# Kernel tuning notes

Hardware: AMD Instinct MI355X
Metric: run time of the kernel (lower is better)

The kernel has to match this reference:

```python
import jax, jax.numpy as jnp
import numpy as np

EPS = 1e-6


def _gru_cell(x, h, w_ih, w_hh, b_ih, b_hh):
    # PyTorch GRU gate order: r, z, n
    gi = x @ w_ih.T + b_ih          # (B, 3H)
    gh = h @ w_hh.T + b_hh          # (B, 3H)
    ir, iz, inn = jnp.split(gi, 3, axis=-1)
    hr, hz, hn = jnp.split(gh, 3, axis=-1)
    r = jax.nn.sigmoid(ir + hr)
    z = jax.nn.sigmoid(iz + hz)
    n = jnp.tanh(inn + r * hn)
    return (1.0 - z) * n + z * h


def setup_inputs() -> dict:
    key = jax.random.key(0)
    B, C, H, O = 32768, 512, 256, 2
    ks = jax.random.split(key, 16)
    s_ih0 = 1.0 / np.sqrt(H)
    inp = {
        "context": jax.random.normal(ks[0], (B, C), dtype=jnp.float32),
        "pred_len": 60,
        "w_init": jax.random.normal(ks[1], (H * 2, C), dtype=jnp.float32) * (1.0 / np.sqrt(C)),
        "b_init": jnp.zeros((H * 2,), dtype=jnp.float32),
        "w_ih0": jax.random.normal(ks[2], (3 * H, O + C), dtype=jnp.float32) * s_ih0,
        "w_hh0": jax.random.normal(ks[3], (3 * H, H), dtype=jnp.float32) * s_ih0,
        "b_ih0": jax.random.normal(ks[4], (3 * H,), dtype=jnp.float32) * s_ih0,
        "b_hh0": jax.random.normal(ks[5], (3 * H,), dtype=jnp.float32) * s_ih0,
        "w_ih1": jax.random.normal(ks[6], (3 * H, H), dtype=jnp.float32) * s_ih0,
        "w_hh1": jax.random.normal(ks[7], (3 * H, H), dtype=jnp.float32) * s_ih0,
        "b_ih1": jax.random.normal(ks[8], (3 * H,), dtype=jnp.float32) * s_ih0,
        "b_hh1": jax.random.normal(ks[9], (3 * H,), dtype=jnp.float32) * s_ih0,
        "w_pos": jax.random.normal(ks[10], (O, H), dtype=jnp.float32) * s_ih0,
        "b_pos": jnp.zeros((O,), dtype=jnp.float32),
        "w_chol": jax.random.normal(ks[11], (3, H), dtype=jnp.float32) * s_ih0,
        "b_chol": jnp.zeros((3,), dtype=jnp.float32),
    }
    return inp


def reference(context, pred_len, w_init, b_init,
              w_ih0, w_hh0, b_ih0, b_hh0,
              w_ih1, w_hh1, b_ih1, b_hh1,
              w_pos, b_pos, w_chol, b_chol):
    B = context.shape[0]
    H = w_hh0.shape[1]
    # init hidden: tanh(W_init c + b), split into per-layer states
    hid = jnp.tanh(context @ w_init.T + b_init)       # (B, 2H)
    h0, h1 = hid[:, :H], hid[:, H:]
    pos0 = jnp.zeros((B, w_pos.shape[0]), dtype=context.dtype)
    zeros = jnp.zeros((B,), dtype=context.dtype)

    def step(carry, _):
        h0, h1, pos = carry
        x = jnp.concatenate([pos, context], axis=1)   # (B, O+C)
        h0 = _gru_cell(x, h0, w_ih0, w_hh0, b_ih0, b_hh0)
        h1 = _gru_cell(h0, h1, w_ih1, w_hh1, b_ih1, b_hh1)
        pred = h1 @ w_pos.T + b_pos                   # (B, 2)
        z = h1 @ w_chol.T + b_chol                    # (B, 3)
        l11 = jax.nn.softplus(z[:, 0]) + EPS
        l21 = z[:, 1]
        l22 = jax.nn.softplus(z[:, 2]) + EPS
        L = jnp.stack([jnp.stack([l11, zeros], axis=-1),
                       jnp.stack([l21, l22], axis=-1)], axis=-2)  # (B, 2, 2)
        return (h0, h1, pred), (pred, L)

    _, (preds, Ls) = jax.lax.scan(step, (h0, h1, pos0), None, length=pred_len)
    predictions = jnp.transpose(preds, (1, 0, 2))     # (B, T, 2)
    cholesky = jnp.transpose(Ls, (1, 0, 2, 3))        # (B, T, 2, 2)
    return predictions, cholesky
```

## Files before the change

### kernel.cpp

```cpp
#include <hip/hip_runtime.h>
#include <hip/hip_bf16.h>
#include <cstdint>
#include <cstddef>


typedef __attribute__((ext_vector_type(8)))  short bf16x8;
typedef __attribute__((ext_vector_type(16))) float f32x16;
typedef __attribute__((ext_vector_type(4)))  float f32x4;
typedef unsigned short ushort_t;
typedef unsigned int   uint32;

#define MFMA_BF16(A,B,C) __builtin_amdgcn_mfma_f32_32x32x16_bf16(A,B,C,0,0,0)
#define MMA3(ACC, AH, AL, BH, BL)            \
  ACC = MFMA_BF16(AH, BH, ACC);              \
  ACC = MFMA_BF16(AH, BL, ACC);              \
  ACC = MFMA_BF16(AL, BH, ACC);

#define TSTEPS 60
#define CB_OFF 3932160

#define WPK0 0u
#define WPK1 786432u
#define WPK2 1572864u
#define WPKI 2359296u
#define WPKG 3407872u
#define JCON 4980736u
#define OUTW 4993024u
#define NTWO 5001216u

#define OFF_H0 0
#define OFF_H1 65536
#define OFF_BUF 131072
#define OFF_POS 147456
#define SMEM_BYTES 147968

__device__ __forceinline__ ushort_t f2bf(float x){
  uint32 u = __builtin_bit_cast(uint32, x);
  u += 0x7fffu + ((u >> 16) & 1u);
  return (ushort_t)(u >> 16);
}
__device__ __forceinline__ float bf2f(ushort_t b){
  uint32 u = ((uint32)b) << 16;
  return __builtin_bit_cast(float, u);
}
__device__ __forceinline__ void zero16(f32x16& a){
  #pragma unroll
  for (int i=0;i<16;i++) a[i] = 0.f;
}

#define LOG2E 1.44269504088896340736f
#define LN2   0.69314718055994530942f
__device__ __forceinline__ float fexp2(float x){ return __builtin_amdgcn_exp2f(x); }
__device__ __forceinline__ float flog2(float x){ return __builtin_amdgcn_logf(x); }
__device__ __forceinline__ float frcp (float x){ return __builtin_amdgcn_rcpf(x); }
__device__ __forceinline__ float fsig(float x){ return frcp(1.f + fexp2(-LOG2E*x)); }
__device__ __forceinline__ float ftanh(float x){
  float ax = fabsf(x);
  float e  = fexp2(-2.f*LOG2E*ax);
  float t  = (1.f - e)*frcp(1.f + e);
  return copysignf(t, x);
}
__device__ __forceinline__ float fsoftplus(float x){
  float ax = fabsf(x);
  return fmaxf(x, 0.f) + LN2*flog2(1.f + fexp2(-LOG2E*ax));
}

__device__ __forceinline__ void pack_unit(const float* __restrict__ src, int stride, int colOff,
                                          char* __restrict__ dst, int NC, int ncLog, int v)
{
  int l = v & 63;
  int c = (v >> 6) & (NC-1);
  int t = v >> (6 + ncLog);
  int j  = 32*t + (l & 31);
  int k0 = 16*c + ((l >> 5) << 3);
  const float* s = src + (size_t)j*stride + colOff + k0;
  uint32 hp[4], lp[4];
  #pragma unroll
  for (int i=0;i<4;i++){
    float x0 = s[2*i], x1 = s[2*i+1];
    ushort_t h0_ = f2bf(x0), h1_ = f2bf(x1);
    ushort_t l0_ = f2bf(x0 - bf2f(h0_)), l1_ = f2bf(x1 - bf2f(h1_));
    hp[i] = (uint32)h0_ | ((uint32)h1_ << 16);
    lp[i] = (uint32)l0_ | ((uint32)l1_ << 16);
  }
  char* d = dst + ((size_t)(t*NC + c))*2048 + (size_t)l*16;
  *(uint4*)d          = make_uint4(hp[0],hp[1],hp[2],hp[3]);
  *(uint4*)(d + 1024) = make_uint4(lp[0],lp[1],lp[2],lp[3]);
}

__global__ void k_pack(const float* __restrict__ w_init, const float* __restrict__ w_ih0,
                       const float* __restrict__ w_hh0, const float* __restrict__ b_hh0,
                       const float* __restrict__ w_ih1, const float* __restrict__ w_hh1,
                       const float* __restrict__ b_ih1, const float* __restrict__ b_hh1,
                       const float* __restrict__ w_pos, const float* __restrict__ w_chol,
                       char* __restrict__ ws)
{
  int u = blockIdx.x*256 + threadIdx.x;
  if (u < 73728){
    int seg = u / 24576; int v = u % 24576;
    const float* src = (seg==0) ? w_hh0 : ((seg==1) ? w_ih1 : w_hh1);
    char* dst = ws + ((seg==0) ? WPK0 : ((seg==1) ? WPK1 : WPK2));
    pack_unit(src, 256, 0, dst, 16, 4, v);
  } else if (u < 106496){
    pack_unit(w_init, 512, 0, ws + WPKI, 32, 5, u - 73728);
  } else if (u < 155648){
    pack_unit(w_ih0, 514, 2, ws + WPKG, 32, 5, u - 106496);
  } else if (u < 156416){
    int j = u - 155648;
    float w4 = (j < 512) ? (b_ih1[j] + b_hh1[j]) : b_ih1[j];
    ((float4*)(ws + JCON))[j] =
        make_float4(b_hh0[j], w_ih0[(size_t)j*514 + 0], w_ih0[(size_t)j*514 + 1], w4);
  } else if (u < 156672){
    int k = u - 156416;
    ((float4*)(ws + OUTW))[2*k]   = make_float4(w_pos[k], w_pos[256+k], w_chol[k], w_chol[256+k]);
    ((float4*)(ws + OUTW))[2*k+1] = make_float4(w_chol[512+k], 0.f, 0.f, 0.f);
  } else if (u < 156928){
    int k = u - 156672;
    ((float*)(ws + NTWO))[k] = b_hh1[512+k];
  }
}


template<int NTILE, int NCHUNK>
__device__ __forceinline__ void gemm_frag(const char* __restrict__ apk, int w, int l,
                                          const char* __restrict__ sbase,
                                          f32x16 (&acc)[NTILE][2])
{
  #pragma unroll 4
  for (int c=0;c<NCHUNK;c++){
    bf16x8 A[NTILE][2];
    #pragma unroll
    for (int i=0;i<NTILE;i++){
      const char* p = apk + ((size_t)((w+8*i)*NCHUNK + c))*2048 + (size_t)l*16;
      A[i][0] = *(const bf16x8*)p;
      A[i][1] = *(const bf16x8*)(p + 1024);
    }
    bf16x8 Bf[2][2];
    #pragma unroll
    for (int s=0;s<2;s++)
      #pragma unroll
      for (int p2=0;p2<2;p2++)
        Bf[s][p2] = *(const bf16x8*)(sbase + ((c*2+p2)*2+s)*1024 + l*16);
    #pragma unroll
    for (int i=0;i<NTILE;i++)
      #pragma unroll
      for (int s=0;s<2;s++){
        MMA3(acc[i][s], A[i][0], A[i][1], Bf[s][0], Bf[s][1]);
      }
  }
}

__device__ __forceinline__ void readback(const char* __restrict__ hbase, int w, int l,
                                         f32x16 (&ho)[2])
{
  const int L = l >> 5, l31 = l & 31;
  #pragma unroll
  for (int s=0;s<2;s++)
    #pragma unroll
    for (int g=0;g<4;g++){
      int cg = 2*w + (g>>1);
      int lane2 = l31 + 32*(g&1);
      const char* ph = hbase + ((cg*2+0)*2 + s)*1024 + lane2*16 + 8*L;
      const char* pl = hbase + ((cg*2+1)*2 + s)*1024 + lane2*16 + 8*L;
      uint2 hb = *(const uint2*)ph;
      uint2 lb = *(const uint2*)pl;
      ho[s][4*g+0] = bf2f((ushort_t)(hb.x & 0xffff)) + bf2f((ushort_t)(lb.x & 0xffff));
      ho[s][4*g+1] = bf2f((ushort_t)(hb.x >> 16))    + bf2f((ushort_t)(lb.x >> 16));
      ho[s][4*g+2] = bf2f((ushort_t)(hb.y & 0xffff)) + bf2f((ushort_t)(lb.y & 0xffff));
      ho[s][4*g+3] = bf2f((ushort_t)(hb.y >> 16))    + bf2f((ushort_t)(lb.y >> 16));
    }
}

__device__ __forceinline__ void write_state(char* __restrict__ hbase, int w, int l,
                                            const f32x16 (&hn)[2])
{
  const int L = l >> 5;
  #pragma unroll
  for (int s=0;s<2;s++){
    float loc[16], sw[16];
    #pragma unroll
    for (int q=0;q<16;q++){ loc[q] = hn[s][q]; sw[q] = __shfl_xor(loc[q], 32, 64); }
    #pragma unroll
    for (int c=0;c<2;c++){
      float v[8];
      if (L == 0){
        #pragma unroll
        for (int r=0;r<8;r++){ int q = (r&3) + 8*c;     v[r] = (r<4)  ? loc[q] : sw[q]; }
      } else {
        #pragma unroll
        for (int r=0;r<8;r++){ int q = (r&3) + 8*c + 4; v[r] = (r>=4) ? loc[q] : sw[q]; }
      }
      uint32 hp[4], lp[4];
      #pragma unroll
      for (int i=0;i<4;i++){
        ushort_t h0_ = f2bf(v[2*i]), h1_ = f2bf(v[2*i+1]);
        ushort_t l0_ = f2bf(v[2*i] - bf2f(h0_)), l1_ = f2bf(v[2*i+1] - bf2f(h1_));
        hp[i] = (uint32)h0_ | ((uint32)h1_ << 16);
        lp[i] = (uint32)l0_ | ((uint32)l1_ << 16);
      }
      int cg = 2*w + c;
      *(uint4*)(hbase + ((cg*2+0)*2+s)*1024 + l*16) = make_uint4(hp[0],hp[1],hp[2],hp[3]);
      *(uint4*)(hbase + ((cg*2+1)*2+s)*1024 + l*16) = make_uint4(lp[0],lp[1],lp[2],lp[3]);
    }
  }
}

__global__ __launch_bounds__(512, 2) void decoder_main(
    const float* __restrict__ ctx,
    const float* __restrict__ b_init,
    const float* __restrict__ b_ih0,
    const float* __restrict__ b_pos,
    const float* __restrict__ b_chol,
    const char*  __restrict__ ws,
    float*       __restrict__ out)
{
  extern __shared__ char smem[];
  const int tid = threadIdx.x;
  const int w   = tid >> 6;
  const int l   = tid & 63;
  const int L   = l >> 5;
  const int l31 = l & 31;
  const int blk = blockIdx.x;
  const int B0  = blk * 64;
  const float4* jconst = (const float4*)(ws + JCON);
  const float4* outw   = (const float4*)(ws + OUTW);
  const float*  n2c    = (const float*)(ws + NTWO);
  float* posb = (float*)(smem + OFF_POS);
  float* buff = (float*)(smem + OFF_BUF);

  #pragma unroll
  for (int ci=0; ci<4; ci++){
    int c = w + 8*ci;
    #pragma unroll
    for (int s=0;s<2;s++){
      const float* src = ctx + (size_t)(B0 + 32*s + l31)*512 + 16*c + 8*L;
      float4 a0 = *(const float4*)src;
      float4 a1 = *(const float4*)(src + 4);
      float xs[8] = {a0.x,a0.y,a0.z,a0.w,a1.x,a1.y,a1.z,a1.w};
      uint32 hp[4], lp[4];
      #pragma unroll
      for (int i=0;i<4;i++){
        ushort_t h0_ = f2bf(xs[2*i]), h1_ = f2bf(xs[2*i+1]);
        ushort_t l0_ = f2bf(xs[2*i] - bf2f(h0_)), l1_ = f2bf(xs[2*i+1] - bf2f(h1_));
        hp[i] = (uint32)h0_ | ((uint32)h1_ << 16);
        lp[i] = (uint32)l0_ | ((uint32)l1_ << 16);
      }
      *(uint4*)(smem + ((c*2+0)*2 + s)*1024 + l*16) = make_uint4(hp[0],hp[1],hp[2],hp[3]);
      *(uint4*)(smem + ((c*2+1)*2 + s)*1024 + l*16) = make_uint4(lp[0],lp[1],lp[2],lp[3]);
    }
  }
  __syncthreads();

  f32x16 hD0[2], hD1[2];
  {
    f32x16 aH[2][2];
    zero16(aH[0][0]); zero16(aH[0][1]); zero16(aH[1][0]); zero16(aH[1][1]);
    gemm_frag<2,32>(ws + WPKI, w, l, smem, aH);
    #pragma unroll
    for (int ti=0; ti<2; ti++)
      #pragma unroll
      for (int s=0;s<2;s++)
        #pragma unroll
        for (int g=0;g<4;g++)
          #pragma unroll
          for (int e=0;e<4;e++){
            int kq = 4*L + e + 8*g;
            int j  = 32*(w + 8*ti) + kq;
            float v = ftanh(aH[ti][s][4*g+e] + b_init[j]);
            if (ti==0) hD0[s][4*g+e] = v; else hD1[s][4*g+e] = v;
          }
  }

  f32x16 gi[3][2];
  {
    #pragma unroll
    for (int i=0;i<3;i++){ zero16(gi[i][0]); zero16(gi[i][1]); }
    gemm_frag<3,32>(ws + WPKG, w, l, smem, gi);
    #pragma unroll
    for (int ti=0; ti<3; ti++)
      #pragma unroll
      for (int s=0;s<2;s++)
        #pragma unroll
        for (int g=0;g<4;g++)
          #pragma unroll
          for (int e=0;e<4;e++){
            int kq = 4*L + e + 8*g;
            int j  = 32*(w + 8*ti) + kq;
            gi[ti][s][4*g+e] += b_ih0[j];
          }
  }
  __syncthreads();

  write_state(smem + OFF_H0, w, l, hD0);
  write_state(smem + OFF_H1, w, l, hD1);
  if (tid < 128) posb[tid] = 0.f;
  __syncthreads();

  for (int t=0; t<TSTEPS; t++){
    f32x16 g0[3][2];
    #pragma unroll
    for (int i=0;i<3;i++){ zero16(g0[i][0]); zero16(g0[i][1]); }
    gemm_frag<3,16>(ws + WPK0, w, l, smem + OFF_H0, g0);

    f32x16 ho[2];
    readback(smem + OFF_H0, w, l, ho);
    float p0v[2], p1v[2];
    #pragma unroll
    for (int s=0;s<2;s++){
      float2 pp = *(const float2*)(posb + (32*s + l31)*2);
      p0v[s] = pp.x; p1v[s] = pp.y;
    }

    f32x16 hn0[2];
    #pragma unroll
    for (int g=0;g<4;g++)
      #pragma unroll
      for (int e=0;e<4;e++){
        int kq = 4*L + e + 8*g;
        int jr = 32*w + kq;
        float4 jcr = jconst[jr], jcz = jconst[256+jr], jcn = jconst[512+jr];
        #pragma unroll
        for (int s=0;s<2;s++){
          int q = 4*g + e;
          float gi_r = gi[0][s][q] + jcr.y*p0v[s] + jcr.z*p1v[s];
          float gi_z = gi[1][s][q] + jcz.y*p0v[s] + jcz.z*p1v[s];
          float gi_n = gi[2][s][q] + jcn.y*p0v[s] + jcn.z*p1v[s];
          float r = fsig(gi_r + g0[0][s][q] + jcr.x);
          float z = fsig(gi_z + g0[1][s][q] + jcz.x);
          float n = ftanh(gi_n + r*(g0[2][s][q] + jcn.x));
          hn0[s][q] = (1.f - z)*n + z*ho[s][q];
        }
      }
    __syncthreads();
    write_state(smem + OFF_H0, w, l, hn0);
    __syncthreads();

    f32x16 aR[2], aZ[2], aNi[2], aNh[2];
    zero16(aR[0]); zero16(aR[1]); zero16(aZ[0]); zero16(aZ[1]);
    zero16(aNi[0]); zero16(aNi[1]); zero16(aNh[0]); zero16(aNh[1]);
    {
      const char* pk1 = ws + WPK1;
      const char* pk2 = ws + WPK2;
      #pragma unroll 4
      for (int c=0;c<16;c++){
        bf16x8 A1[3][2], A2[3][2];
        #pragma unroll
        for (int i=0;i<3;i++){
          size_t o = ((size_t)((w+8*i)*16 + c))*2048 + (size_t)l*16;
          A1[i][0] = *(const bf16x8*)(pk1+o); A1[i][1] = *(const bf16x8*)(pk1+o+1024);
          A2[i][0] = *(const bf16x8*)(pk2+o); A2[i][1] = *(const bf16x8*)(pk2+o+1024);
        }
        bf16x8 B0f[2][2], B1f[2][2];
        #pragma unroll
        for (int s=0;s<2;s++)
          #pragma unroll
          for (int p2=0;p2<2;p2++){
            B0f[s][p2] = *(const bf16x8*)(smem + OFF_H0 + ((c*2+p2)*2+s)*1024 + l*16);
            B1f[s][p2] = *(const bf16x8*)(smem + OFF_H1 + ((c*2+p2)*2+s)*1024 + l*16);
          }
        #pragma unroll
        for (int s=0;s<2;s++){
          MMA3(aR[s],  A1[0][0], A1[0][1], B0f[s][0], B0f[s][1]);
          MMA3(aR[s],  A2[0][0], A2[0][1], B1f[s][0], B1f[s][1]);
          MMA3(aZ[s],  A1[1][0], A1[1][1], B0f[s][0], B0f[s][1]);
          MMA3(aZ[s],  A2[1][0], A2[1][1], B1f[s][0], B1f[s][1]);
          MMA3(aNi[s], A1[2][0], A1[2][1], B0f[s][0], B0f[s][1]);
          MMA3(aNh[s], A2[2][0], A2[2][1], B1f[s][0], B1f[s][1]);
        }
      }
    }

    f32x16 h1o[2];
    readback(smem + OFF_H1, w, l, h1o);
    f32x16 hn1[2];
    #pragma unroll
    for (int g=0;g<4;g++)
      #pragma unroll
      for (int e=0;e<4;e++){
        int kq = 4*L + e + 8*g;
        int k  = 32*w + kq;
        float4 jcr = jconst[k], jcz = jconst[256+k], jcn = jconst[512+k];
        float nb = n2c[k];
        #pragma unroll
        for (int s=0;s<2;s++){
          int q = 4*g + e;
          float r = fsig(aR[s][q] + jcr.w);
          float z = fsig(aZ[s][q] + jcz.w);
          float n = ftanh(aNi[s][q] + jcn.w + r*(aNh[s][q] + nb));
          hn1[s][q] = (1.f - z)*n + z*h1o[s][q];
        }
      }
    __syncthreads();
    write_state(smem + OFF_H1, w, l, hn1);

    float part[2][5];
    #pragma unroll
    for (int s=0;s<2;s++){ part[s][0]=part[s][1]=part[s][2]=part[s][3]=part[s][4]=0.f; }
    #pragma unroll
    for (int g=0;g<4;g++)
      #pragma unroll
      for (int e=0;e<4;e++){
        int kq = 4*L + e + 8*g;
        int k  = 32*w + kq;
        float4 o0 = outw[2*k], o1 = outw[2*k+1];
        #pragma unroll
        for (int s=0;s<2;s++){
          float h = hn1[s][4*g+e];
          part[s][0] += h*o0.x; part[s][1] += h*o0.y; part[s][2] += h*o0.z;
          part[s][3] += h*o0.w; part[s][4] += h*o1.x;
        }
      }
    #pragma unroll
    for (int s=0;s<2;s++)
      #pragma unroll
      for (int o=0;o<5;o++)
        part[s][o] += __shfl_xor(part[s][o], 32, 64);
    if (l < 32){
      #pragma unroll
      for (int s=0;s<2;s++){
        float* bp = buff + (size_t)(w*64 + 32*s + l)*8;
        bp[0]=part[s][0]; bp[1]=part[s][1]; bp[2]=part[s][2]; bp[3]=part[s][3]; bp[4]=part[s][4];
      }
    }
    __syncthreads();

    if (tid < 320){
      int b = tid / 5, o = tid - 5*b;
      float v = 0.f;
      #pragma unroll
      for (int w8=0; w8<8; w8++) v += buff[(size_t)(w8*64 + b)*8 + o];
      int gb = B0 + b;
      if (o < 2){
        float pr = v + b_pos[o];
        out[(size_t)gb*120 + t*2 + o] = pr;
        posb[b*2 + o] = pr;
      } else if (o == 2){
        float l11 = fsoftplus(v + b_chol[0]) + 1e-6f;
        out[CB_OFF + (size_t)gb*240 + t*4 + 0] = l11;
        out[CB_OFF + (size_t)gb*240 + t*4 + 1] = 0.f;
      } else if (o == 3){
        out[CB_OFF + (size_t)gb*240 + t*4 + 2] = v + b_chol[1];
      } else {
        out[CB_OFF + (size_t)gb*240 + t*4 + 3] = fsoftplus(v + b_chol[2]) + 1e-6f;
      }
    }
    __syncthreads();
  }
}

extern "C" void kernel_launch(void* const* d_in, const int* in_sizes, int n_in,
                              void* d_out, int out_size, void* d_ws, size_t ws_size,
                              hipStream_t stream)
{
  const float* ctx    = (const float*)d_in[0];
  const float* w_init = (const float*)d_in[2];
  const float* b_init = (const float*)d_in[3];
  const float* w_ih0  = (const float*)d_in[4];
  const float* w_hh0  = (const float*)d_in[5];
  const float* b_ih0  = (const float*)d_in[6];
  const float* b_hh0  = (const float*)d_in[7];
  const float* w_ih1  = (const float*)d_in[8];
  const float* w_hh1  = (const float*)d_in[9];
  const float* b_ih1  = (const float*)d_in[10];
  const float* b_hh1  = (const float*)d_in[11];
  const float* w_pos  = (const float*)d_in[12];
  const float* b_pos  = (const float*)d_in[13];
  const float* w_chol = (const float*)d_in[14];
  const float* b_chol = (const float*)d_in[15];
  char*  ws  = (char*)d_ws;
  float* out = (float*)d_out;

  hipFuncSetAttribute((const void*)decoder_main,
                      hipFuncAttributeMaxDynamicSharedMemorySize, SMEM_BYTES);

  k_pack<<<613, 256, 0, stream>>>(w_init, w_ih0, w_hh0, b_hh0, w_ih1, w_hh1,
                                  b_ih1, b_hh1, w_pos, w_chol, ws);
  decoder_main<<<512, 512, SMEM_BYTES, stream>>>(ctx, b_init, b_ih0, b_pos, b_chol,
                                                 ws, out);
}
```

Measured before the change: 13.17 ms.

## Pack loop-invariant input gates to fp16 and split layer-1 GEMM to cut registers

The precomputed input-gate accumulators (gi), which live in registers across all timesteps, are now stored as packed fp16 pairs, halving their register footprint. The layer-1 recurrent GEMM is split into two passes: r/z gates first, whose sigmoid outputs are packed to fp16, then the n-gate accumulators. This lowers peak accumulator liveness. Unroll factors drop from 4 to 2 to further reduce register pressure, likely aiming to avoid spills or raise occupancy. In exchange it adds fp16 rounding of the gate values, extra pack/unpack work, and a second pass over the hidden state in LDS.

```diff
diff --git a/kernel.cpp b/kernel.cpp
--- a/kernel.cpp
+++ b/kernel.cpp
@@ -1,5 +1,6 @@
 #include <hip/hip_runtime.h>
 #include <hip/hip_bf16.h>
+#include <hip/hip_fp16.h>
 #include <cstdint>
 #include <cstddef>
 
@@ -46,6 +47,15 @@
 __device__ __forceinline__ void zero16(f32x16& a){
   #pragma unroll
   for (int i=0;i<16;i++) a[i] = 0.f;
+}
+__device__ __forceinline__ uint32 packh2(float a, float b){
+  ushort_t ua = __builtin_bit_cast(ushort_t, __float2half_rn(a));
+  ushort_t ub = __builtin_bit_cast(ushort_t, __float2half_rn(b));
+  return (uint32)ua | ((uint32)ub << 16);
+}
+__device__ __forceinline__ float unph(uint32 p, int hiHalf){
+  ushort_t u = (ushort_t)(hiHalf ? (p >> 16) : (p & 0xffffu));
+  return __half2float(__builtin_bit_cast(__half, u));
 }
 
 #define LOG2E 1.44269504088896340736f
@@ -126,7 +136,7 @@
                                           const char* __restrict__ sbase,
                                           f32x16 (&acc)[NTILE][2])
 {
-  #pragma unroll 4
+  #pragma unroll 2
   for (int c=0;c<NCHUNK;c++){
     bf16x8 A[NTILE][2];
     #pragma unroll
@@ -251,6 +261,27 @@
   }
   __syncthreads();
 
+  uint32 giP[3][2][8];
+  {
+    f32x16 aG[3][2];
+    #pragma unroll
+    for (int i=0;i<3;i++){ zero16(aG[i][0]); zero16(aG[i][1]); }
+    gemm_frag<3,32>(ws + WPKG, w, l, smem, aG);
+    #pragma unroll
+    for (int ti=0; ti<3; ti++)
+      #pragma unroll
+      for (int s=0;s<2;s++)
+        #pragma unroll
+        for (int j=0;j<8;j++){
+          int q0 = 2*j, q1 = 2*j+1;
+          int kq0 = 4*L + (q0&3) + 8*(q0>>2);
+          int kq1 = 4*L + (q1&3) + 8*(q1>>2);
+          float v0 = aG[ti][s][q0] + b_ih0[32*(w+8*ti) + kq0];
+          float v1 = aG[ti][s][q1] + b_ih0[32*(w+8*ti) + kq1];
+          giP[ti][s][j] = packh2(v0, v1);
+        }
+  }
+
   f32x16 hD0[2], hD1[2];
   {
     f32x16 aH[2][2];
@@ -270,25 +301,6 @@
             if (ti==0) hD0[s][4*g+e] = v; else hD1[s][4*g+e] = v;
           }
   }
-
-  f32x16 gi[3][2];
-  {
-    #pragma unroll
-    for (int i=0;i<3;i++){ zero16(gi[i][0]); zero16(gi[i][1]); }
-    gemm_frag<3,32>(ws + WPKG, w, l, smem, gi);
-    #pragma unroll
-    for (int ti=0; ti<3; ti++)
-      #pragma unroll
-      for (int s=0;s<2;s++)
-        #pragma unroll
-        for (int g=0;g<4;g++)
-          #pragma unroll
-          for (int e=0;e<4;e++){
-            int kq = 4*L + e + 8*g;
-            int j  = 32*(w + 8*ti) + kq;
-            gi[ti][s][4*g+e] += b_ih0[j];
-          }
-  }
   __syncthreads();
 
   write_state(smem + OFF_H0, w, l, hD0);
@@ -318,13 +330,13 @@
       for (int e=0;e<4;e++){
         int kq = 4*L + e + 8*g;
         int jr = 32*w + kq;
+        int q  = 4*g + e;
         float4 jcr = jconst[jr], jcz = jconst[256+jr], jcn = jconst[512+jr];
         #pragma unroll
         for (int s=0;s<2;s++){
-          int q = 4*g + e;
-          float gi_r = gi[0][s][q] + jcr.y*p0v[s] + jcr.z*p1v[s];
-          float gi_z = gi[1][s][q] + jcz.y*p0v[s] + jcz.z*p1v[s];
-          float gi_n = gi[2][s][q] + jcn.y*p0v[s] + jcn.z*p1v[s];
+          float gi_r = unph(giP[0][s][q>>1], q&1) + jcr.y*p0v[s] + jcr.z*p1v[s];
+          float gi_z = unph(giP[1][s][q>>1], q&1) + jcz.y*p0v[s] + jcz.z*p1v[s];
+          float gi_n = unph(giP[2][s][q>>1], q&1) + jcn.y*p0v[s] + jcn.z*p1v[s];
           float r = fsig(gi_r + g0[0][s][q] + jcr.x);
           float z = fsig(gi_z + g0[1][s][q] + jcz.x);
           float n = ftanh(gi_n + r*(g0[2][s][q] + jcn.x));
@@ -335,17 +347,17 @@
     write_state(smem + OFF_H0, w, l, hn0);
     __syncthreads();
 
-    f32x16 aR[2], aZ[2], aNi[2], aNh[2];
-    zero16(aR[0]); zero16(aR[1]); zero16(aZ[0]); zero16(aZ[1]);
-    zero16(aNi[0]); zero16(aNi[1]); zero16(aNh[0]); zero16(aNh[1]);
+    uint32 rP[2][8], zP[2][8];
     {
+      f32x16 aR[2], aZ[2];
+      zero16(aR[0]); zero16(aR[1]); zero16(aZ[0]); zero16(aZ[1]);
       const char* pk1 = ws + WPK1;
       const char* pk2 = ws + WPK2;
-      #pragma unroll 4
+      #pragma unroll 2
       for (int c=0;c<16;c++){
-        bf16x8 A1[3][2], A2[3][2];
-        #pragma unroll
-        for (int i=0;i<3;i++){
+        bf16x8 A1[2][2], A2[2][2];
+        #pragma unroll
+        for (int i=0;i<2;i++){
           size_t o = ((size_t)((w+8*i)*16 + c))*2048 + (size_t)l*16;
           A1[i][0] = *(const bf16x8*)(pk1+o); A1[i][1] = *(const bf16x8*)(pk1+o+1024);
           A2[i][0] = *(const bf16x8*)(pk2+o); A2[i][1] = *(const bf16x8*)(pk2+o+1024);
@@ -360,36 +372,77 @@
           }
         #pragma unroll
         for (int s=0;s<2;s++){
-          MMA3(aR[s],  A1[0][0], A1[0][1], B0f[s][0], B0f[s][1]);
-          MMA3(aR[s],  A2[0][0], A2[0][1], B1f[s][0], B1f[s][1]);
-          MMA3(aZ[s],  A1[1][0], A1[1][1], B0f[s][0], B0f[s][1]);
-          MMA3(aZ[s],  A2[1][0], A2[1][1], B1f[s][0], B1f[s][1]);
-          MMA3(aNi[s], A1[2][0], A1[2][1], B0f[s][0], B0f[s][1]);
-          MMA3(aNh[s], A2[2][0], A2[2][1], B1f[s][0], B1f[s][1]);
-        }
-      }
-    }
-
-    f32x16 h1o[2];
-    readback(smem + OFF_H1, w, l, h1o);
+          MMA3(aR[s], A1[0][0], A1[0][1], B0f[s][0], B0f[s][1]);
+          MMA3(aR[s], A2[0][0], A2[0][1], B1f[s][0], B1f[s][1]);
+          MMA3(aZ[s], A1[1][0], A1[1][1], B0f[s][0], B0f[s][1]);
+          MMA3(aZ[s], A2[1][0], A2[1][1], B1f[s][0], B1f[s][1]);
+        }
+      }
+      #pragma unroll
+      for (int s=0;s<2;s++)
+        #pragma unroll
+        for (int j=0;j<8;j++){
+          int q0 = 2*j, q1 = 2*j+1;
+          int k0 = 32*w + 4*L + (q0&3) + 8*(q0>>2);
+          int k1 = 32*w + 4*L + (q1&3) + 8*(q1>>2);
+          float r0 = fsig(aR[s][q0] + jconst[k0].w);
+          float r1 = fsig(aR[s][q1] + jconst[k1].w);
+          float z0 = fsig(aZ[s][q0] + jconst[256+k0].w);
+          float z1 = fsig(aZ[s][q1] + jconst[256+k1].w);
+          rP[s][j] = packh2(r0, r1);
+          zP[s][j] = packh2(z0, z1);
+        }
+    }
+
     f32x16 hn1[2];
-    #pragma unroll
-    for (int g=0;g<4;g++)
-      #pragma unroll
-      for (int e=0;e<4;e++){
-        int kq = 4*L + e + 8*g;
-        int k  = 32*w + kq;
-        float4 jcr = jconst[k], jcz = jconst[256+k], jcn = jconst[512+k];
-        float nb = n2c[k];
+    {
+      f32x16 aNi[2], aNh[2];
+      zero16(aNi[0]); zero16(aNi[1]); zero16(aNh[0]); zero16(aNh[1]);
+      const char* pk1 = ws + WPK1;
+      const char* pk2 = ws + WPK2;
+      #pragma unroll 2
+      for (int c=0;c<16;c++){
+        bf16x8 A1f[2], A2f[2];
+        {
+          size_t o = ((size_t)((w+16)*16 + c))*2048 + (size_t)l*16;
+          A1f[0] = *(const bf16x8*)(pk1+o); A1f[1] = *(const bf16x8*)(pk1+o+1024);
+          A2f[0] = *(const bf16x8*)(pk2+o); A2f[1] = *(const bf16x8*)(pk2+o+1024);
+        }
+        bf16x8 B0f[2][2], B1f[2][2];
+        #pragma unroll
+        for (int s=0;s<2;s++)
+          #pragma unroll
+          for (int p2=0;p2<2;p2++){
+            B0f[s][p2] = *(const bf16x8*)(smem + OFF_H0 + ((c*2+p2)*2+s)*1024 + l*16);
+            B1f[s][p2] = *(const bf16x8*)(smem + OFF_H1 + ((c*2+p2)*2+s)*1024 + l*16);
+          }
         #pragma unroll
         for (int s=0;s<2;s++){
-          int q = 4*g + e;
-          float r = fsig(aR[s][q] + jcr.w);
-          float z = fsig(aZ[s][q] + jcz.w);
-          float n = ftanh(aNi[s][q] + jcn.w + r*(aNh[s][q] + nb));
-          hn1[s][q] = (1.f - z)*n + z*h1o[s][q];
-        }
-      }
+          MMA3(aNi[s], A1f[0], A1f[1], B0f[s][0], B0f[s][1]);
+          MMA3(aNh[s], A2f[0], A2f[1], B1f[s][0], B1f[s][1]);
+        }
+      }
+
+      f32x16 h1o[2];
+      readback(smem + OFF_H1, w, l, h1o);
+      #pragma unroll
+      for (int g=0;g<4;g++)
+        #pragma unroll
+        for (int e=0;e<4;e++){
+          int kq = 4*L + e + 8*g;
+          int k  = 32*w + kq;
+          int q  = 4*g + e;
+          float jcnw = jconst[512+k].w;
+          float nb   = n2c[k];
+          #pragma unroll
+          for (int s=0;s<2;s++){
+            float r = unph(rP[s][q>>1], q&1);
+            float z = unph(zP[s][q>>1], q&1);
+            float n = ftanh(aNi[s][q] + jcnw + r*(aNh[s][q] + nb));
+            hn1[s][q] = (1.f - z)*n + z*h1o[s][q];
+          }
+        }
+    }
     __syncthreads();
     write_state(smem + OFF_H1, w, l, hn1);
 
```

New measurement: 14.00 ms. 6.3% more time.
